# Kernel tuning notes

Measured on AMD Instinct MI355X. Metric: run time of the kernel, lower is better.

The kernel has to match this reference:

```python
import jax, jax.numpy as jnp
import numpy as np

N_NODES, N_EDGES, N_GRAPHS = 8192, 32768, 256
FXD, HEADS = 78, 10
D2 = FXD * HEADS  # 780
FF = 2048
L_MUT = 735
NF = 32
OUT_DIM = 128


def _ln(x, g, b, eps=1e-5):
    m = x.mean(-1, keepdims=True)
    v = ((x - m) ** 2).mean(-1, keepdims=True)
    return (x - m) * jax.lax.rsqrt(v + eps) * g + b


def _transformer(x, in_w, in_b, out_w, out_b, ln1_g, ln1_b, l1_w, l1_b, l2_w, l2_b, ln2_g, ln2_b):
    # post-LN TransformerEncoderLayer, nhead=1, seq = all N nodes, batch = 1 (eval: dropout off)
    E = x.shape[-1]
    q, k, v = jnp.split(x @ in_w.T + in_b, 3, axis=-1)
    a = jax.nn.softmax((q @ k.T) * (1.0 / np.sqrt(E)), axis=-1) @ v  # [N,N] scores
    x = _ln(x + a @ out_w.T + out_b, ln1_g, ln1_b)
    h = jax.nn.relu(x @ l1_w.T + l1_b) @ l2_w.T + l2_b
    return _ln(x + h, ln2_g, ln2_b)


def _gat(x, src, dst, w, a_src, a_dst, bias):
    # PyG GATConv, heads=10, concat=True, leaky 0.2, self loops already in src/dst
    N = x.shape[0]
    h = (x @ w.T).reshape(N, HEADS, FXD)
    asrc = (h * a_src).sum(-1)  # [N,H]
    adst = (h * a_dst).sum(-1)
    alpha = jax.nn.leaky_relu(asrc[src] + adst[dst], 0.2)  # [E,H]
    amax = jax.lax.stop_gradient(jax.ops.segment_max(alpha, dst, num_segments=N))
    ex = jnp.exp(alpha - amax[dst])
    coef = ex / (jax.ops.segment_sum(ex, dst, num_segments=N)[dst] + 1e-16)
    out = jax.ops.segment_sum(coef[:, :, None] * h[src], dst, num_segments=N)
    return out.reshape(N, HEADS * FXD) + bias


def _gcn(x, src, dst, w, b):
    # PyG GCNConv with self loops (already in src/dst), symmetric norm
    N = x.shape[0]
    deg = jax.ops.segment_sum(jnp.ones(dst.shape, x.dtype), dst, num_segments=N)
    dis = jnp.where(deg > 0, jax.lax.rsqrt(jnp.maximum(deg, 1.0)), 0.0)
    norm = dis[src] * dis[dst]
    return jax.ops.segment_sum(norm[:, None] * (x @ w.T)[src], dst, num_segments=N) + b


def _conv1d(x, w, b):
    y = jax.lax.conv_general_dilated(x, w, (1,), 'VALID', dimension_numbers=('NCH', 'OIH', 'NCH'))
    return y + b[None, :, None]


def _convT1d(x, w, b):
    # torch ConvTranspose1d weight [in,out,k] -> flipped [out,in,k], full padding
    k = w.shape[-1]
    ker = jnp.flip(w, -1).transpose(1, 0, 2)
    y = jax.lax.conv_general_dilated(x, ker, (1,), [(k - 1, k - 1)], dimension_numbers=('NCH', 'OIH', 'NCH'))
    return y + b[None, :, None]


def _maxpool1d(x, k):
    return jax.lax.reduce_window(x, -jnp.inf, jax.lax.max, (1, 1, k), (1, 1, k), 'VALID')


def _bn_eval(x, g, b, eps=1e-5):
    # eval-mode BatchNorm1d with fresh running stats (mean 0, var 1)
    return x * (g / np.sqrt(1.0 + eps))[None, :, None] + b[None, :, None]


def _forward(edge_index, batch, x, target_mut, t1_in_w, t1_in_b, t1_out_w, t1_out_b, t1_ln1_g, t1_ln1_b, t1_l1_w, t1_l1_b, t1_l2_w, t1_l2_b, t1_ln2_g, t1_ln2_b, gat_w, gat_asrc, gat_adst, gat_b, t2_in_w, t2_in_b, t2_out_w, t2_out_b, t2_ln1_g, t2_ln1_b, t2_l1_w, t2_l1_b, t2_l2_w, t2_l2_b, t2_ln2_g, t2_ln2_b, gcn_w, gcn_b, fcg1_w, fcg1_b, fcg2_w, fcg2_b, e1_w, e1_b, bn1_g, bn1_b, e2_w, e2_b, bn2_g, bn2_b, e3_w, e3_b, enc_lin_w, enc_lin_b, d3_w, d3_b, dbn2_g, dbn2_b, d2_w, d2_b, dbn1_g, dbn1_b, d1_w, d1_b, fc1_w, fc1_b, fc2_w, fc2_b, out_w, out_b):
    N = x.shape[0]
    xg = _transformer(x, t1_in_w, t1_in_b, t1_out_w, t1_out_b, t1_ln1_g, t1_ln1_b, t1_l1_w, t1_l1_b, t1_l2_w, t1_l2_b, t1_ln2_g, t1_ln2_b)
    loops = jnp.arange(N, dtype=edge_index.dtype)
    src = jnp.concatenate([edge_index[0], loops])
    dst = jnp.concatenate([edge_index[1], loops])
    xg = jax.nn.relu(_gat(xg, src, dst, gat_w, gat_asrc, gat_adst, gat_b))
    xg = _transformer(xg, t2_in_w, t2_in_b, t2_out_w, t2_out_b, t2_ln1_g, t2_ln1_b, t2_l1_w, t2_l1_b, t2_l2_w, t2_l2_b, t2_ln2_g, t2_ln2_b)
    xg = jax.nn.relu(_gcn(xg, src, dst, gcn_w, gcn_b))
    gm = jax.ops.segment_max(xg, batch, num_segments=N_GRAPHS)
    gm = jnp.where(jnp.isfinite(gm), gm, 0.0)
    cnt = jax.ops.segment_sum(jnp.ones((N,), xg.dtype), batch, num_segments=N_GRAPHS)
    ga = jax.ops.segment_sum(xg, batch, num_segments=N_GRAPHS) / jnp.maximum(cnt, 1.0)[:, None]
    xd = jnp.concatenate([gm, ga], axis=1)  # [B, 1560]
    xd = jax.nn.relu(xd @ fcg1_w.T + fcg1_b)
    xd = xd @ fcg2_w.T + fcg2_b  # [B, 128]
    # conv1d autoencoder on mutation profile
    t = target_mut[:, None, :]  # [B,1,735]
    e = jax.nn.leaky_relu(_bn_eval(_maxpool1d(_conv1d(t, e1_w, e1_b), 8), bn1_g, bn1_b))
    e = jax.nn.leaky_relu(_bn_eval(_maxpool1d(_conv1d(e, e2_w, e2_b), 7), bn2_g, bn2_b))
    e = _conv1d(e, e3_w, e3_b)  # [B,128,5]
    z = e.reshape(e.shape[0], -1) @ enc_lin_w.T + enc_lin_b  # [B,128]
    d = jnp.repeat(jax.nn.leaky_relu(_bn_eval(_convT1d(e, d3_w, d3_b), dbn2_g, dbn2_b)), 7, axis=-1)
    d = jnp.repeat(jax.nn.leaky_relu(_bn_eval(_convT1d(d, d2_w, d2_b), dbn1_g, dbn1_b)), 8, axis=-1)
    decode = _convT1d(d, d1_w, d1_b)  # [B,1,735]
    xc = jnp.concatenate([xd, z], axis=1)
    xc = jax.nn.relu(xc @ fc1_w.T + fc1_b)
    xc = jax.nn.relu(xc @ fc2_w.T + fc2_b)
    out = jax.nn.sigmoid(xc @ out_w.T + out_b)
    return (out, xd, decode)


def setup_inputs():
    key = jax.random.key(0)
    ks = iter(jax.random.split(key, 64))

    def rn(*shape):
        return jax.random.normal(next(ks), shape, jnp.float32) * 0.05

    inp = {}
    inp['x'] = jax.random.normal(next(ks), (N_NODES, FXD), jnp.float32)
    inp['edge_index'] = jax.random.randint(next(ks), (2, N_EDGES), 0, N_NODES)
    inp['batch'] = jnp.sort(jax.random.randint(next(ks), (N_NODES,), 0, N_GRAPHS))
    inp['target_mut'] = jax.random.normal(next(ks), (N_GRAPHS, L_MUT), jnp.float32)
    for p, E in (('t1', FXD), ('t2', D2)):
        inp[p + '_in_w'] = rn(3 * E, E); inp[p + '_in_b'] = jnp.zeros((3 * E,))
        inp[p + '_out_w'] = rn(E, E); inp[p + '_out_b'] = jnp.zeros((E,))
        inp[p + '_ln1_g'] = jnp.ones((E,)); inp[p + '_ln1_b'] = jnp.zeros((E,))
        inp[p + '_l1_w'] = rn(FF, E); inp[p + '_l1_b'] = jnp.zeros((FF,))
        inp[p + '_l2_w'] = rn(E, FF); inp[p + '_l2_b'] = jnp.zeros((E,))
        inp[p + '_ln2_g'] = jnp.ones((E,)); inp[p + '_ln2_b'] = jnp.zeros((E,))
    inp['gat_w'] = rn(D2, FXD); inp['gat_asrc'] = rn(HEADS, FXD); inp['gat_adst'] = rn(HEADS, FXD); inp['gat_b'] = jnp.zeros((D2,))
    inp['gcn_w'] = rn(D2, D2); inp['gcn_b'] = jnp.zeros((D2,))
    inp['fcg1_w'] = rn(1500, 2 * D2); inp['fcg1_b'] = jnp.zeros((1500,))
    inp['fcg2_w'] = rn(OUT_DIM, 1500); inp['fcg2_b'] = jnp.zeros((OUT_DIM,))
    inp['e1_w'] = rn(NF, 1, 8); inp['e1_b'] = jnp.zeros((NF,))
    inp['bn1_g'] = jnp.ones((NF,)); inp['bn1_b'] = jnp.zeros((NF,))
    inp['e2_w'] = rn(2 * NF, NF, 8); inp['e2_b'] = jnp.zeros((2 * NF,))
    inp['bn2_g'] = jnp.ones((2 * NF,)); inp['bn2_b'] = jnp.zeros((2 * NF,))
    inp['e3_w'] = rn(4 * NF, 2 * NF, 8); inp['e3_b'] = jnp.zeros((4 * NF,))
    inp['enc_lin_w'] = rn(OUT_DIM, 640); inp['enc_lin_b'] = jnp.zeros((OUT_DIM,))
    inp['d3_w'] = rn(4 * NF, 2 * NF, 8); inp['d3_b'] = jnp.zeros((2 * NF,))
    inp['dbn2_g'] = jnp.ones((2 * NF,)); inp['dbn2_b'] = jnp.zeros((2 * NF,))
    inp['d2_w'] = rn(2 * NF, NF, 8); inp['d2_b'] = jnp.zeros((NF,))
    inp['dbn1_g'] = jnp.ones((NF,)); inp['dbn1_b'] = jnp.zeros((NF,))
    inp['d1_w'] = rn(NF, 1, 8); inp['d1_b'] = jnp.zeros((1,))
    inp['fc1_w'] = rn(1024, 2 * OUT_DIM); inp['fc1_b'] = jnp.zeros((1024,))
    inp['fc2_w'] = rn(128, 1024); inp['fc2_b'] = jnp.zeros((128,))
    inp['out_w'] = rn(1, 128); inp['out_b'] = jnp.zeros((1,))
    return inp


def reference(x, edge_index, batch, target_mut, t1_in_w, t1_in_b, t1_out_w, t1_out_b, t1_ln1_g, t1_ln1_b, t1_l1_w, t1_l1_b, t1_l2_w, t1_l2_b, t1_ln2_g, t1_ln2_b, gat_w, gat_asrc, gat_adst, gat_b, t2_in_w, t2_in_b, t2_out_w, t2_out_b, t2_ln1_g, t2_ln1_b, t2_l1_w, t2_l1_b, t2_l2_w, t2_l2_b, t2_ln2_g, t2_ln2_b, gcn_w, gcn_b, fcg1_w, fcg1_b, fcg2_w, fcg2_b, e1_w, e1_b, bn1_g, bn1_b, e2_w, e2_b, bn2_g, bn2_b, e3_w, e3_b, enc_lin_w, enc_lin_b, d3_w, d3_b, dbn2_g, dbn2_b, d2_w, d2_b, dbn1_g, dbn1_b, d1_w, d1_b, fc1_w, fc1_b, fc2_w, fc2_b, out_w, out_b):
    return _forward(edge_index, batch, x, target_mut, t1_in_w, t1_in_b, t1_out_w, t1_out_b, t1_ln1_g, t1_ln1_b, t1_l1_w, t1_l1_b, t1_l2_w, t1_l2_b, t1_ln2_g, t1_ln2_b, gat_w, gat_asrc, gat_adst, gat_b, t2_in_w, t2_in_b, t2_out_w, t2_out_b, t2_ln1_g, t2_ln1_b, t2_l1_w, t2_l1_b, t2_l2_w, t2_l2_b, t2_ln2_g, t2_ln2_b, gcn_w, gcn_b, fcg1_w, fcg1_b, fcg2_w, fcg2_b, e1_w, e1_b, bn1_g, bn1_b, e2_w, e2_b, bn2_g, bn2_b, e3_w, e3_b, enc_lin_w, enc_lin_b, d3_w, d3_b, dbn2_g, dbn2_b, d2_w, d2_b, dbn1_g, dbn1_b, d1_w, d1_b, fc1_w, fc1_b, fc2_w, fc2_b, out_w, out_b)
```

## Files before the change

### kernel.cpp

```cpp
#include <hip/hip_runtime.h>
#include <math.h>

#define NN     8192
#define NEDGE  32768
#define NETOT  40960
#define NG     256
#define FXD_   78
#define NH     10
#define DD2    780
#define FFD    2048
#define LMUT   735

static inline int cdiv_i(long long a, int b){ return (int)((a + (long long)b - 1) / b); }
static inline int pad32(int x){ return (x + 31) & ~31; }

typedef __attribute__((ext_vector_type(8))) short bf16x8;
typedef __attribute__((ext_vector_type(4))) float f32x4;

static __device__ __forceinline__ unsigned short f2bf(float f){
    unsigned u = __float_as_uint(f);
    u += 0x7FFFu + ((u >> 16) & 1u);
    return (unsigned short)(u >> 16);
}

static __device__ __forceinline__ void gload16(const void* g, void* l){
    __builtin_amdgcn_global_load_lds((const __attribute__((address_space(1))) void*)g,
                                     (__attribute__((address_space(3))) void*)l, 16, 0, 0);
}

__global__ void fill_f32_k(float* __restrict__ p, float v, long long n){
    long long i = (long long)blockIdx.x * 256 + threadIdx.x;
    if (i < n) p[i] = v;
}
__global__ void fill_u32_k(unsigned* __restrict__ p, unsigned v, long long n){
    long long i = (long long)blockIdx.x * 256 + threadIdx.x;
    if (i < n) p[i] = v;
}

__global__ void cvt_pad_k(const float* __restrict__ src, unsigned short* __restrict__ dst,
                          long long n , int C, int lds_, int ldd)
{
    long long i = (long long)blockIdx.x * 256 + threadIdx.x;
    if (i >= n) return;
    int r = (int)(i / ldd), c = (int)(i % ldd);
    dst[i] = (c < C) ? f2bf(src[(size_t)r * lds_ + c]) : (unsigned short)0;
}

__global__ void norm_cvt_k(const float* __restrict__ A4, unsigned short* __restrict__ XB,
                           int E, int Ep)
{
    long long i = (long long)blockIdx.x * 256 + threadIdx.x;
    if (i >= (long long)NN * Ep) return;
    int r = (int)(i / Ep), c = (int)(i % Ep);
    XB[i] = (c < E) ? f2bf(A4[(size_t)r * Ep + c] / A4[(size_t)r * Ep + E]) : (unsigned short)0;
}

__global__ void tr_bf16_k(const unsigned short* __restrict__ src, unsigned short* __restrict__ dst,
                          int R, int C, int lds_, int ldd)
{
    __shared__ unsigned short t[32][33];
    int cb = blockIdx.x * 32, rb = blockIdx.y * 32;
    int tx = threadIdx.x & 31, ty = threadIdx.x >> 5;
#pragma unroll
    for (int i = 0; i < 4; ++i){
        int r = rb + ty + i * 8, c = cb + tx;
        t[ty + i * 8][tx] = (r < R && c < C) ? src[(size_t)r * lds_ + c] : (unsigned short)0;
    }
    __syncthreads();
#pragma unroll
    for (int i = 0; i < 4; ++i){
        int dr = cb + ty + i * 8, dc = rb + tx;
        if (dr < C && dc < R) dst[(size_t)dr * ldd + dc] = t[tx][ty + i * 8];
    }
}

__global__ void qkv_bias_k(const float* __restrict__ b3, float* __restrict__ out, int E, int Ep)
{
    int idx = blockIdx.x * 256 + threadIdx.x;
    if (idx >= 3 * Ep) return;
    int s = idx / Ep, c = idx % Ep;
    out[idx] = (c < E) ? b3[s * E + c] : 0.f;
}

__global__ void bias_add_k(float* __restrict__ X, const float* __restrict__ b, long long n, int cols)
{
    long long i = (long long)blockIdx.x * 256 + threadIdx.x;
    if (i < n) X[i] += b[i % cols];
}

template<int OUTC, int ACT, int SPLITK, int BROW, int BN>
__global__ __launch_bounds__(256) void mgemm_k(
    const unsigned short* __restrict__ A, const unsigned short* __restrict__ B,
    const float* __restrict__ bias, void* __restrict__ Cv,
    int M, int N, int Kp, int lda, int ldb, int ldc, int swz, float escale)
{
    constexpr int NFJ   = BN / 32;
    constexpr int TILEA = 128 * 32;
    constexpr int TILEB = BN * 32;
    __shared__ unsigned short As[2 * TILEA];
    __shared__ unsigned short Bs[2 * TILEB];
    const int tid = threadIdx.x;
    const int lane = tid & 63, wid = tid >> 6;
    const int r16 = lane & 15, q = lane >> 4;
    const int wr = (wid >> 1) * 64, wc = (wid & 1) * (BN / 2);

    const int gx = gridDim.x, gy = gridDim.y;
    const int nwg = gx * gy;
    int orig = swz ? ((int)blockIdx.x * gy + (int)blockIdx.y)
                   : ((int)blockIdx.y * gx + (int)blockIdx.x);
    int q8 = nwg >> 3, r8 = nwg & 7;
    int xcd = orig & 7, kk8 = orig >> 3;
    int wgid = (xcd < r8 ? xcd * (q8 + 1) : r8 * (q8 + 1) + (xcd - r8) * q8) + kk8;
    int bx, by;
    if (swz){ by = wgid % gy; bx = wgid / gy; }
    else    { bx = wgid % gx; by = wgid / gx; }
    const int row0 = by * 128, col0 = bx * BN;

    int kbeg = 0, kend = Kp;
    if (SPLITK > 1){
        int nt_ = Kp >> 5, cpt = (nt_ + SPLITK - 1) / SPLITK;
        kbeg = (int)blockIdx.z * cpt * 32;
        kend = min(Kp, kbeg + cpt * 32);
    }

    const int c0 = wid * 128 + lane;
    const int r0a = c0 >> 2, k0a = (c0 & 3) << 3;
    const size_t gA0 = (size_t)min(row0 + r0a, M - 1) * lda + k0a;
    const size_t gA1 = (size_t)min(row0 + r0a + 16, M - 1) * lda + k0a;
    unsigned short* lA = As + wid * 1024;
    size_t gB0 = 0, gB1 = 0;
    unsigned short* lB;
    if (BN == 128){
        gB0 = (size_t)min(col0 + r0a, N - 1) * ldb + k0a;
        gB1 = (size_t)min(col0 + r0a + 16, N - 1) * ldb + k0a;
        lB = Bs + wid * 1024;
    } else {
        const int cb = wid * 64 + lane;
        const int rb_ = cb >> 2, kb_ = (cb & 3) << 3;
        gB0 = (size_t)min(col0 + rb_, N - 1) * ldb + kb_;
        lB = Bs + wid * 512;
    }

    f32x4 acc[4][NFJ];
#pragma unroll
    for (int i = 0; i < 4; ++i)
#pragma unroll
        for (int j = 0; j < NFJ; ++j){ f32x4 z = {0.f, 0.f, 0.f, 0.f}; acc[i][j] = z; }

    const int nt = (kend - kbeg) >> 5;
    if (nt > 0){
        gload16(A + gA0 + kbeg, lA);
        gload16(A + gA1 + kbeg, lA + 512);
        gload16(B + gB0 + kbeg, lB);
        if (BN == 128) gload16(B + gB1 + kbeg, lB + 512);
        __syncthreads();
        int cur = 0;
        for (int t = 0; t < nt; ++t){
            const int k0 = kbeg + (t << 5);
            if (t + 1 < nt){
                const int kn = k0 + 32, nb = cur ^ 1;
                gload16(A + gA0 + kn, lA + nb * TILEA);
                gload16(A + gA1 + kn, lA + nb * TILEA + 512);
                gload16(B + gB0 + kn, lB + nb * TILEB);
                if (BN == 128) gload16(B + gB1 + kn, lB + nb * TILEB + 512);
            }
            const unsigned short* Ab = As + cur * TILEA;
            const unsigned short* Bb = Bs + cur * TILEB;
            bf16x8 af[4], bfv[NFJ];
#pragma unroll
            for (int f = 0; f < 4; ++f)
                af[f] = *(const bf16x8*)(Ab + (size_t)(wr + f * 16 + r16) * 32 + (q << 3));
#pragma unroll
            for (int f = 0; f < NFJ; ++f)
                bfv[f] = *(const bf16x8*)(Bb + (size_t)(wc + f * 16 + r16) * 32 + (q << 3));
#pragma unroll
            for (int fi = 0; fi < 4; ++fi)
#pragma unroll
                for (int fj = 0; fj < NFJ; ++fj)
                    acc[fi][fj] = __builtin_amdgcn_mfma_f32_16x16x32_bf16(af[fi], bfv[fj], acc[fi][fj], 0, 0, 0);
            __syncthreads();
            cur ^= 1;
        }
    }

    if (OUTC == 1 && SPLITK == 1 && row0 + 128 <= M && col0 + BN <= N && (ldc & 7) == 0){
#pragma unroll
        for (int fi = 0; fi < 4; ++fi)
#pragma unroll
            for (int fj = 0; fj < NFJ; ++fj)
#pragma unroll
                for (int j = 0; j < 4; ++j){
                    int r = wr + fi * 16 + q * 4 + j;
                    int c = wc + fj * 16 + r16;
                    float v = acc[fi][fj][j];
                    if (bias) v += BROW ? bias[row0 + r] : bias[col0 + c];
                    if (ACT == 1) v = fmaxf(v, 0.f);
                    if (ACT == 2) v = 1.f / (1.f + __expf(-v));
                    if (ACT == 3) v = __expf(v * escale);
                    unsigned short* buf = (r < 64) ? As : Bs;
                    buf[(r & 63) * BN + (c ^ ((r & 7) << 3))] = f2bf(v);
                }
        __syncthreads();
        const int CPR = BN / 8;
        for (int id = tid; id < 128 * CPR; id += 256){
            int r = id / CPR, cg = (id % CPR) * 8;
            const unsigned short* buf = (r < 64) ? As : Bs;
            uint4 vv = *(const uint4*)(&buf[(r & 63) * BN + (cg ^ ((r & 7) << 3))]);
            *(uint4*)((unsigned short*)Cv + (size_t)(row0 + r) * ldc + col0 + cg) = vv;
        }
        return;
    }

#pragma unroll
    for (int fi = 0; fi < 4; ++fi){
#pragma unroll
        for (int j = 0; j < 4; ++j){
            int r = row0 + wr + fi * 16 + q * 4 + j;
            if (r >= M) continue;
#pragma unroll
            for (int fj = 0; fj < NFJ; ++fj){
                int c = col0 + wc + fj * 16 + r16;
                if (c >= N) continue;
                float v = acc[fi][fj][j];
                if (SPLITK > 1){
                    atomicAdd((float*)Cv + (size_t)r * ldc + c, v);
                } else {
                    if (bias) v += BROW ? bias[r] : bias[c];
                    if (ACT == 1) v = fmaxf(v, 0.f);
                    if (ACT == 2) v = 1.f / (1.f + __expf(-v));
                    if (ACT == 3) v = __expf(v * escale);
                    if (OUTC == 0) ((float*)Cv)[(size_t)r * ldc + c] = v;
                    else ((unsigned short*)Cv)[(size_t)r * ldc + c] = f2bf(v);
                }
            }
        }
    }
}

template<int OUTC, int ACT, int SPLITK, int BROW, int BN>
static void mgemm(hipStream_t s, const unsigned short* A, const unsigned short* B,
                  const float* bias, void* C, int M, int N, int Kp,
                  int lda, int ldb, int ldc, int swz, float escale = 1.f)
{
    dim3 g(cdiv_i(N, BN), cdiv_i(M, 128), SPLITK);
    mgemm_k<OUTC, ACT, SPLITK, BROW, BN><<<g, 256, 0, s>>>(A, B, bias, C, M, N, Kp, lda, ldb, ldc, swz, escale);
}

#define E3P1 288
#define KLD  104
__global__ __launch_bounds__(256) void flash_t1_k(
    const unsigned short* __restrict__ QKV,
    const unsigned short* __restrict__ Vt,
    float* __restrict__ A4, float scale)
{
    __shared__ unsigned short Ps[128 * 128];
    __shared__ unsigned short Vs[80 * 128];
    const int tid = threadIdx.x, lane = tid & 63, wid = tid >> 6;
    const int r16 = lane & 15, q = lane >> 4;
    const int wr = (wid >> 1) * 64;
    const int sc = (wid & 1) * 64;
    const int oc = (wid & 1) * 48;
    const int NJMAX = (wid & 1) ? 2 : 3;
    const int qb = (int)blockIdx.x * 128;
    const int kb = (int)blockIdx.y * 512;

    bf16x8 qa[4][3];
#pragma unroll
    for (int mi = 0; mi < 4; ++mi)
#pragma unroll
        for (int kc = 0; kc < 3; ++kc)
            qa[mi][kc] = *(const bf16x8*)(QKV + (size_t)(qb + wr + mi * 16 + r16) * E3P1 + kc * 32 + (q << 3));

    f32x4 acco[4][3];
#pragma unroll
    for (int i = 0; i < 4; ++i)
#pragma unroll
        for (int j = 0; j < 3; ++j){ f32x4 z = {0.f, 0.f, 0.f, 0.f}; acco[i][j] = z; }

    for (int t = 0; t < 4; ++t){
        const int k0 = kb + t * 128;
#pragma unroll
        for (int i = 0; i < 6; ++i){
            int id = tid + i * 256;
            int row = id / 12, co = (id % 12) << 3;
            *(bf16x8*)(&Ps[row * KLD + co]) =
                *(const bf16x8*)(QKV + (size_t)(k0 + row) * E3P1 + 96 + co);
        }
        __syncthreads();
        f32x4 accs[4][4];
#pragma unroll
        for (int i = 0; i < 4; ++i)
#pragma unroll
            for (int j = 0; j < 4; ++j){ f32x4 z = {0.f, 0.f, 0.f, 0.f}; accs[i][j] = z; }
#pragma unroll
        for (int kc = 0; kc < 3; ++kc){
            bf16x8 bk[4];
#pragma unroll
            for (int nj = 0; nj < 4; ++nj)
                bk[nj] = *(const bf16x8*)(&Ps[(sc + nj * 16 + r16) * KLD + kc * 32 + (q << 3)]);
#pragma unroll
            for (int mi = 0; mi < 4; ++mi)
#pragma unroll
                for (int nj = 0; nj < 4; ++nj)
                    accs[mi][nj] = __builtin_amdgcn_mfma_f32_16x16x32_bf16(qa[mi][kc], bk[nj], accs[mi][nj], 0, 0, 0);
        }
        __syncthreads();
#pragma unroll
        for (int mi = 0; mi < 4; ++mi)
#pragma unroll
            for (int nj = 0; nj < 4; ++nj)
#pragma unroll
                for (int j = 0; j < 4; ++j){
                    int row = wr + mi * 16 + q * 4 + j;
                    int col = sc + nj * 16 + r16;
                    Ps[row * 128 + (col ^ ((row & 7) << 3))] = f2bf(__expf(accs[mi][nj][j] * scale));
                }
#pragma unroll
        for (int i = 0; i < 5; ++i){
            int id = tid + i * 256;
            int row = id / 16, co = (id % 16) << 3;
            *(bf16x8*)(&Vs[row * 128 + (co ^ ((row & 7) << 3))]) =
                *(const bf16x8*)(Vt + (size_t)row * NN + k0 + co);
        }
        __syncthreads();
#pragma unroll
        for (int ko = 0; ko < 4; ++ko){
            bf16x8 pa[4], vb[3];
#pragma unroll
            for (int mi = 0; mi < 4; ++mi){
                int row = wr + mi * 16 + r16;
                pa[mi] = *(const bf16x8*)(&Ps[row * 128 + ((ko * 32 + (q << 3)) ^ ((row & 7) << 3))]);
            }
#pragma unroll
            for (int nj = 0; nj < 3; ++nj){
                if (nj < NJMAX){
                    int row = oc + nj * 16 + r16;
                    vb[nj] = *(const bf16x8*)(&Vs[row * 128 + ((ko * 32 + (q << 3)) ^ ((row & 7) << 3))]);
                }
            }
#pragma unroll
            for (int mi = 0; mi < 4; ++mi)
#pragma unroll
                for (int nj = 0; nj < 3; ++nj)
                    if (nj < NJMAX)
                        acco[mi][nj] = __builtin_amdgcn_mfma_f32_16x16x32_bf16(pa[mi], vb[nj], acco[mi][nj], 0, 0, 0);
        }
        __syncthreads();
    }
#pragma unroll
    for (int mi = 0; mi < 4; ++mi)
#pragma unroll
        for (int j = 0; j < 4; ++j){
            int r = qb + wr + mi * 16 + q * 4 + j;
#pragma unroll
            for (int nj = 0; nj < 3; ++nj){
                if (nj < NJMAX){
                    int c = oc + nj * 16 + r16;
                    if (c <= FXD_)
                        atomicAdd(A4 + (size_t)r * 96 + c, acco[mi][nj][j]);
                }
            }
        }
}

__global__ __launch_bounds__(256) void add_ln_k(
    const float* __restrict__ X, const float* __restrict__ Y, const float* __restrict__ ybias,
    const float* __restrict__ g, const float* __restrict__ b,
    float* __restrict__ out, unsigned short* __restrict__ obf, int E, int Ep)
{
    __shared__ float s1[256], s2[256];
    const int tid = threadIdx.x;
    long long base = (long long)blockIdx.x * E;
    float vals[4];
    float sum = 0.f, sq = 0.f;
    int i = 0;
    for (int c = tid; c < Ep; c += 256, ++i){
        float v = 0.f;
        if (c < E){
            v = X[base + c] + Y[base + c];
            if (ybias) v += ybias[c];
            sum += v; sq += v * v;
        }
        vals[i] = v;
    }
    s1[tid] = sum; s2[tid] = sq; __syncthreads();
    for (int s = 128; s; s >>= 1){
        if (tid < s){ s1[tid] += s1[tid + s]; s2[tid] += s2[tid + s]; }
        __syncthreads();
    }
    float mean = s1[0] / (float)E;
    float var = s2[0] / (float)E - mean * mean;
    if (var < 0.f) var = 0.f;
    float inv = 1.f / sqrtf(var + 1e-5f);
    i = 0;
    for (int c = tid; c < Ep; c += 256, ++i){
        if (c < E){
            float o = (vals[i] - mean) * inv * g[c] + b[c];
            out[base + c] = o;
            if (obf) obf[(size_t)blockIdx.x * Ep + c] = f2bf(o);
        } else if (obf) obf[(size_t)blockIdx.x * Ep + c] = 0;
    }
}

static __device__ __forceinline__ unsigned enc_f(float x){
    unsigned u = __float_as_uint(x);
    return (u & 0x80000000u) ? ~u : (u | 0x80000000u);
}
static __device__ __forceinline__ float dec_f(unsigned u){
    return (u & 0x80000000u) ? __uint_as_float(u & 0x7fffffffu) : __uint_as_float(~u);
}
static __device__ __forceinline__ void edge_sd(const int* __restrict__ ei, int e, int& s, int& d){
    if (e < NEDGE){ s = ei[e]; d = ei[NEDGE + e]; }
    else { s = e - NEDGE; d = e - NEDGE; }
}

__global__ void gat_srcdst_k(const float* __restrict__ h, const float* __restrict__ aw_src,
                             const float* __restrict__ aw_dst, float* __restrict__ asrc,
                             float* __restrict__ adst)
{
    int idx = blockIdx.x * 256 + threadIdx.x;
    if (idx >= NN * NH) return;
    int n = idx / NH, hh = idx % NH;
    const float* hp = h + (long long)n * DD2 + hh * FXD_;
    const float* ws = aw_src + hh * FXD_;
    const float* wd = aw_dst + hh * FXD_;
    float s1 = 0.f, s2 = 0.f;
    for (int f = 0; f < FXD_; ++f){ float v = hp[f]; s1 += v * ws[f]; s2 += v * wd[f]; }
    asrc[idx] = s1; adst[idx] = s2;
}

__global__ void gat_alpha_k(const int* __restrict__ ei, const float* __restrict__ asrc,
                            const float* __restrict__ adst, float* __restrict__ alpha,
                            unsigned* __restrict__ amax)
{
    int idx = blockIdx.x * 256 + threadIdx.x;
    if (idx >= NETOT * NH) return;
    int e = idx / NH, hh = idx % NH;
    int s, d; edge_sd(ei, e, s, d);
    float a = asrc[s * NH + hh] + adst[d * NH + hh];
    a = (a > 0.f) ? a : 0.2f * a;
    alpha[idx] = a;
    atomicMax(&amax[d * NH + hh], enc_f(a));
}

__global__ void gat_expsum_k(const int* __restrict__ ei, float* __restrict__ alpha,
                             const unsigned* __restrict__ amax, float* __restrict__ denom)
{
    int idx = blockIdx.x * 256 + threadIdx.x;
    if (idx >= NETOT * NH) return;
    int e = idx / NH, hh = idx % NH;
    int s, d; edge_sd(ei, e, s, d);
    float m = dec_f(amax[d * NH + hh]);
    float ex = expf(alpha[idx] - m);
    alpha[idx] = ex;
    atomicAdd(&denom[d * NH + hh], ex);
}

__global__ void deg_count_k(const int* __restrict__ ei, int* __restrict__ deg)
{
    int e = blockIdx.x * 256 + threadIdx.x;
    if (e >= NETOT) return;
    int s, d; edge_sd(ei, e, s, d);
    atomicAdd(&deg[d], 1);
}

__global__ __launch_bounds__(256) void csr_off_k(const int* __restrict__ deg,
                                                 int* __restrict__ off, int* __restrict__ cur)
{
    __shared__ int pref[257];
    const int tid = threadIdx.x;
    int loc[32];
    int base = tid * 32, sum = 0;
#pragma unroll
    for (int i = 0; i < 32; ++i){ loc[i] = sum; sum += deg[base + i]; }
    __shared__ int part[256];
    part[tid] = sum; __syncthreads();
    if (tid == 0){
        pref[0] = 0;
        for (int i = 0; i < 256; ++i) pref[i + 1] = pref[i] + part[i];
    }
    __syncthreads();
    int p0 = pref[tid];
#pragma unroll
    for (int i = 0; i < 32; ++i){ off[base + i] = p0 + loc[i]; cur[base + i] = p0 + loc[i]; }
    if (tid == 0) off[NN] = pref[256];
}

__global__ void csr_fill_k(const int* __restrict__ ei, int* __restrict__ cur,
                           int* __restrict__ csr_s, int* __restrict__ csr_e)
{
    int e = blockIdx.x * 256 + threadIdx.x;
    if (e >= NETOT) return;
    int s, d; edge_sd(ei, e, s, d);
    int pos = atomicAdd(&cur[d], 1);
    csr_s[pos] = s; csr_e[pos] = e;
}

__global__ __launch_bounds__(256) void gat_gather_k(
    const int* __restrict__ off, const int* __restrict__ csr_s, const int* __restrict__ csr_e,
    const float* __restrict__ ex, const float* __restrict__ denom,
    const float* __restrict__ hfeat, float* __restrict__ out)
{
    const int d = blockIdx.x, tid = threadIdx.x;
    const int beg = off[d], end = off[d + 1];
    for (int f = tid; f < DD2; f += 256){
        int hh = f / FXD_;
        float acc = 0.f;
        for (int p = beg; p < end; ++p)
            acc += ex[csr_e[p] * NH + hh] * hfeat[(size_t)csr_s[p] * DD2 + f];
        out[(size_t)d * DD2 + f] = acc / (denom[d * NH + hh] + 1e-16f);
    }
}

__global__ __launch_bounds__(256) void gcn_gather_k(
    const int* __restrict__ off, const int* __restrict__ csr_s,
    const float* __restrict__ dis, const float* __restrict__ xw, float* __restrict__ out)
{
    const int d = blockIdx.x, tid = threadIdx.x;
    const int beg = off[d], end = off[d + 1];
    const float dd_ = dis[d];
    for (int f = tid; f < DD2; f += 256){
        float acc = 0.f;
        for (int p = beg; p < end; ++p){
            int s = csr_s[p];
            acc += dis[s] * xw[(size_t)s * DD2 + f];
        }
        out[(size_t)d * DD2 + f] = acc * dd_;
    }
}

__global__ void bias_relu_k(float* __restrict__ X, const float* __restrict__ b,
                            unsigned short* __restrict__ obf, int rows, int cols, int ldp)
{
    long long i = (long long)blockIdx.x * 256 + threadIdx.x;
    if (i >= (long long)rows * ldp) return;
    int r = (int)(i / ldp), c = (int)(i % ldp);
    if (c < cols){
        float v = X[(size_t)r * cols + c] + b[c];
        v = v > 0.f ? v : 0.f;
        X[(size_t)r * cols + c] = v;
        if (obf) obf[i] = f2bf(v);
    } else if (obf) obf[i] = 0;
}

__global__ void dis_k(const int* __restrict__ deg, float* __restrict__ dis)
{
    int n = blockIdx.x * 256 + threadIdx.x;
    if (n >= NN) return;
    float d = (float)deg[n];
    dis[n] = (d > 0.f) ? 1.f / sqrtf(fmaxf(d, 1.f)) : 0.f;
}

__global__ void seg_start_k(const int* __restrict__ batch, int* __restrict__ start)
{
    int n = blockIdx.x * 256 + threadIdx.x;
    if (n >= NN) return;
    int b = batch[n];
    int bp = (n == 0) ? -1 : batch[n - 1];
    for (int g = bp + 1; g <= b; ++g) start[g] = n;
    if (n == NN - 1){
        for (int g = b + 1; g <= NG; ++g) start[g] = NN;
    }
}

__global__ __launch_bounds__(256) void pool_seg_k(const float* __restrict__ xg,
                                                  const int* __restrict__ start,
                                                  unsigned short* __restrict__ xdb)
{
    const int g = blockIdx.x, tid = threadIdx.x;
    const int s0 = start[g], s1 = start[g + 1];
    const float inv = 1.f / fmaxf((float)(s1 - s0), 1.f);
    for (int f = tid; f < DD2; f += 256){
        float mx = 0.f, sm = 0.f;
        for (int n = s0; n < s1; ++n){
            float v = xg[(size_t)n * DD2 + f];
            mx = fmaxf(mx, v); sm += v;
        }
        xdb[(size_t)g * 1568 + f] = f2bf(mx);
        xdb[(size_t)g * 1568 + DD2 + f] = f2bf(sm * inv);
    }
    if (tid < 8) xdb[(size_t)g * 1568 + 1560 + tid] = 0;
}

#define BN_SCALE 0.9999950000374996f

__global__ __launch_bounds__(256) void enc1_b(const float* __restrict__ tm, const float* __restrict__ w,
                                              const float* __restrict__ bias, const float* __restrict__ bng,
                                              const float* __restrict__ bnb, float* __restrict__ out)
{
    __shared__ float xs[736];
    __shared__ float ws[256], bs[32], gs[32], b2[32];
    const int g = blockIdx.x, tid = threadIdx.x;
    for (int i = tid; i < 735; i += 256) xs[i] = tm[(size_t)g * LMUT + i];
    ws[tid] = w[tid];
    if (tid < 32){ bs[tid] = bias[tid]; gs[tid] = bng[tid]; b2[tid] = bnb[tid]; }
    __syncthreads();
    for (int idx = tid; idx < 32 * 91; idx += 256){
        int o = idx / 91, t = idx % 91;
        float mx = -3.4e38f;
        for (int p = 0; p < 8; ++p){
            float s = bs[o];
#pragma unroll
            for (int k = 0; k < 8; ++k) s += xs[t * 8 + p + k] * ws[o * 8 + k];
            mx = fmaxf(mx, s);
        }
        float v = mx * gs[o] * BN_SCALE + b2[o];
        out[(size_t)g * 2912 + idx] = v > 0.f ? v : 0.01f * v;
    }
}

__global__ void i2c_enc2_k(const float* __restrict__ in, unsigned short* __restrict__ A){
    int idx = blockIdx.x * 256 + threadIdx.x;
    if (idx >= NG * 84 * 256) return;
    int col = idx & 255, row = idx >> 8;
    int g = row / 84, u = row % 84;
    int i = col >> 3, k = col & 7;
    A[idx] = f2bf(in[(size_t)g * 2912 + i * 91 + u + k]);
}
__global__ void post_enc2_k(const float* __restrict__ G, const float* __restrict__ b,
                            const float* __restrict__ bng, const float* __restrict__ bnb,
                            float* __restrict__ out){
    int idx = blockIdx.x * 256 + threadIdx.x;
    if (idx >= NG * 768) return;
    int t = idx % 12, o = (idx / 12) & 63, g = idx / 768;
    float mx = -3.4e38f;
#pragma unroll
    for (int p = 0; p < 7; ++p) mx = fmaxf(mx, G[(size_t)(g * 84 + t * 7 + p) * 64 + o]);
    float v = (mx + b[o]) * bng[o] * BN_SCALE + bnb[o];
    out[(size_t)g * 768 + o * 12 + t] = v > 0.f ? v : 0.01f * v;
}
__global__ void i2c_enc3_k(const float* __restrict__ in, unsigned short* __restrict__ A){
    int idx = blockIdx.x * 256 + threadIdx.x;
    if (idx >= NG * 5 * 512) return;
    int col = idx & 511, row = idx >> 9;
    int g = row / 5, t = row % 5;
    int i2 = col >> 3, k = col & 7;
    A[idx] = f2bf(in[(size_t)g * 768 + i2 * 12 + t + k]);
}
__global__ void post_enc3_k(const float* __restrict__ G, const float* __restrict__ b,
                            float* __restrict__ e3o, unsigned short* __restrict__ obf){
    int idx = blockIdx.x * 256 + threadIdx.x;
    if (idx >= NG * 640) return;
    int t = idx % 5, o = (idx / 5) & 127, g = idx / 640;
    float v = G[(size_t)(g * 5 + t) * 128 + o] + b[o];
    e3o[(size_t)g * 640 + o * 5 + t] = v;
    obf[(size_t)g * 640 + o * 5 + t] = f2bf(v);
}
__global__ void wshuf_k(const float* __restrict__ src, unsigned short* __restrict__ dst, int I, int O){
    int idx = blockIdx.x * 256 + threadIdx.x;
    if (idx >= I * O * 8) return;
    int o = idx / (I * 8), rem = idx % (I * 8);
    int i = rem >> 3, j = rem & 7;
    dst[idx] = f2bf(src[(size_t)(i * O + o) * 8 + j]);
}
__global__ void i2c_dec3_k(const float* __restrict__ e3o, unsigned short* __restrict__ A){
    int idx = blockIdx.x * 256 + threadIdx.x;
    if (idx >= NG * 12 * 1024) return;
    int col = idx & 1023, row = idx >> 10;
    int g = row / 12, t = row % 12;
    int i2 = col >> 3, j = col & 7;
    int tt = t - j;
    A[idx] = (tt >= 0 && tt < 5) ? f2bf(e3o[(size_t)g * 640 + i2 * 5 + tt]) : (unsigned short)0;
}
__global__ void post_dec3_k(const float* __restrict__ G, const float* __restrict__ b,
                            const float* __restrict__ bng, const float* __restrict__ bnb,
                            float* __restrict__ dd3){
    int idx = blockIdx.x * 256 + threadIdx.x;
    if (idx >= NG * 768) return;
    int t = idx % 12, o = (idx / 12) & 63, g = idx / 768;
    float v = (G[(size_t)(g * 12 + t) * 64 + o] + b[o]) * bng[o] * BN_SCALE + bnb[o];
    dd3[(size_t)g * 768 + o * 12 + t] = v > 0.f ? v : 0.01f * v;
}
__global__ void i2c_dec2_k(const float* __restrict__ dd3, unsigned short* __restrict__ A){
    int idx = blockIdx.x * 256 + threadIdx.x;
    if (idx >= NG * 91 * 512) return;
    int col = idx & 511, row = idx >> 9;
    int g = row / 91, t = row % 91;
    int i2 = col >> 3, j = col & 7;
    int tt = t - j;
    A[idx] = (tt >= 0 && tt < 84) ? f2bf(dd3[(size_t)g * 768 + i2 * 12 + tt / 7]) : (unsigned short)0;
}
__global__ void post_dec2_k(const float* __restrict__ G, const float* __restrict__ b,
                            const float* __restrict__ bng, const float* __restrict__ bnb,
                            float* __restrict__ dd2){
    int idx = blockIdx.x * 256 + threadIdx.x;
    if (idx >= NG * 2912) return;
    int t = idx % 91, o = (idx / 91) & 31, g = idx / 2912;
    float v = (G[(size_t)(g * 91 + t) * 32 + o] + b[o]) * bng[o] * BN_SCALE + bnb[o];
    dd2[(size_t)g * 2912 + o * 91 + t] = v > 0.f ? v : 0.01f * v;
}

__global__ __launch_bounds__(256) void dec1_b(const float* __restrict__ dd2, const float* __restrict__ w,
                                              const float* __restrict__ bias, float* __restrict__ out)
{
    __shared__ float d2s[32][91];
    __shared__ float ws[256];
    const int g = blockIdx.x, tid = threadIdx.x;
    const int t0 = (int)blockIdx.y * 245;
    for (int i = tid; i < 32 * 91; i += 256) d2s[i / 91][i % 91] = dd2[(size_t)g * 2912 + i];
    ws[tid] = w[tid];
    __syncthreads();
    if (tid < 245){
        int t = t0 + tid;
        int id8[8]; bool ok[8];
#pragma unroll
        for (int j = 0; j < 8; ++j){
            int tt = t - j;
            ok[j] = (tt >= 0 && tt < 728);
            id8[j] = ok[j] ? (tt >> 3) : 0;
        }
        float s = bias[0];
        for (int i2 = 0; i2 < 32; ++i2){
            const float* wp = ws + i2 * 8;
            float a = 0.f;
#pragma unroll
            for (int j = 0; j < 8; ++j) if (ok[j]) a += d2s[i2][id8[j]] * wp[j];
            s += a;
        }
        out[(size_t)g * 735 + t] = s;
    }
}

__global__ void concat_xc_k(const float* __restrict__ xd, const float* __restrict__ z,
                            unsigned short* __restrict__ xcb)
{
    int idx = blockIdx.x * 256 + threadIdx.x;
    if (idx >= NG * 256) return;
    int g = idx >> 8, c = idx & 255;
    xcb[idx] = f2bf((c < 128) ? xd[g * 128 + c] : z[g * 128 + (c - 128)]);
}

extern "C" void kernel_launch(void* const* d_in, const int* in_sizes, int n_in,
                              void* d_out, int out_size, void* d_ws, size_t ws_size,
                              hipStream_t stream)
{
    (void)in_sizes; (void)n_in; (void)out_size;

    const float* x      = (const float*)d_in[0];
    const int*   ei     = (const int*)  d_in[1];
    const int*   batch  = (const int*)  d_in[2];
    const float* tmut   = (const float*)d_in[3];
    const float* t1w[12]; for (int i = 0; i < 12; ++i) t1w[i] = (const float*)d_in[4 + i];
    const float* t2w[12]; for (int i = 0; i < 12; ++i) t2w[i] = (const float*)d_in[16 + i];
    const float* gat_w    = (const float*)d_in[28];
    const float* gat_asrc = (const float*)d_in[29];
    const float* gat_adst = (const float*)d_in[30];
    const float* gat_b    = (const float*)d_in[31];
    const float* gcn_w  = (const float*)d_in[32];
    const float* gcn_b  = (const float*)d_in[33];
    const float* fcg1_w = (const float*)d_in[34];
    const float* fcg1_b = (const float*)d_in[35];
    const float* fcg2_w = (const float*)d_in[36];
    const float* fcg2_b = (const float*)d_in[37];
    const float* e1_w = (const float*)d_in[38]; const float* e1_b = (const float*)d_in[39];
    const float* bn1_g = (const float*)d_in[40]; const float* bn1_b = (const float*)d_in[41];
    const float* e2_w = (const float*)d_in[42]; const float* e2_b = (const float*)d_in[43];
    const float* bn2_g = (const float*)d_in[44]; const float* bn2_b = (const float*)d_in[45];
    const float* e3_w = (const float*)d_in[46]; const float* e3_b = (const float*)d_in[47];
    const float* enc_w = (const float*)d_in[48]; const float* enc_b = (const float*)d_in[49];
    const float* d3_w = (const float*)d_in[50]; const float* d3_b = (const float*)d_in[51];
    const float* dbn2_g = (const float*)d_in[52]; const float* dbn2_b = (const float*)d_in[53];
    const float* d2_w = (const float*)d_in[54]; const float* d2_b = (const float*)d_in[55];
    const float* dbn1_g = (const float*)d_in[56]; const float* dbn1_b = (const float*)d_in[57];
    const float* d1_w = (const float*)d_in[58]; const float* d1_b = (const float*)d_in[59];
    const float* fc1_w = (const float*)d_in[60]; const float* fc1_b = (const float*)d_in[61];
    const float* fc2_w = (const float*)d_in[62]; const float* fc2_b = (const float*)d_in[63];
    const float* outw = (const float*)d_in[64]; const float* outb = (const float*)d_in[65];

    float *A1, *A2, *A3, *A4, *X1f, *QBIASf;
    unsigned short *XB, *QKVb, *Vt, *HbPb;
    unsigned short *WQKVb, *WOUTb, *WL1b, *WL2b, *WGb, *WGCNb, *WFCG1b, *WFCG2b,
                   *WENCb, *WFC1b, *WFC2b, *WOUTWb, *XD16, *FG1b, *E3b, *XCb, *FH1b, *FH2b, *Wcvb;
    float *asrc, *adst, *alpha, *denom, *dis, *c1p, *c2p, *e3o, *zz, *dd3, *dd2b;
    unsigned *amax; int *deg, *seg, *csr_off, *csr_cur, *csr_s, *csr_e;

    auto carve = [&](long long RB) -> size_t {
        char* wp_ = (char*)d_ws;
        auto alc = [&](size_t bytes) -> char* {
            char* p = wp_;
            wp_ += (bytes + 255) & ~(size_t)255;
            return p;
        };
        A1 = (float*)alc((size_t)NN * DD2 * 4);
        A2 = (float*)alc((size_t)NN * DD2 * 4);
        A3 = (float*)alc((size_t)NN * DD2 * 4);
        A4 = (float*)alc((size_t)NN * 800 * 4);
        X1f = (float*)alc((size_t)NN * FXD_ * 4);
        XB   = (unsigned short*)alc((size_t)NN * 800 * 2);
        QKVb = (unsigned short*)alc((size_t)NN * 2400 * 2);
        Vt   = (unsigned short*)alc((size_t)801 * NN * 2);
        size_t hb = (size_t)NN * FFD * 2, pb = (size_t)RB * NN * 2;
        HbPb = (unsigned short*)alc(hb > pb ? hb : pb);
        WQKVb = (unsigned short*)alc((size_t)2400 * 800 * 2);
        QBIASf= (float*)alc((size_t)2400 * 4);
        WOUTb = (unsigned short*)alc((size_t)780 * 800 * 2);
        WL1b  = (unsigned short*)alc((size_t)2048 * 800 * 2);
        WL2b  = (unsigned short*)alc((size_t)780 * 2048 * 2);
        WGb   = (unsigned short*)alc((size_t)780 * 96 * 2);
        WGCNb = (unsigned short*)alc((size_t)780 * 800 * 2);
        WFCG1b= (unsigned short*)alc((size_t)1500 * 1568 * 2);
        WFCG2b= (unsigned short*)alc((size_t)128 * 1504 * 2);
        WENCb = (unsigned short*)alc((size_t)128 * 640 * 2);
        WFC1b = (unsigned short*)alc((size_t)1024 * 256 * 2);
        WFC2b = (unsigned short*)alc((size_t)128 * 1024 * 2);
        WOUTWb= (unsigned short*)alc((size_t)128 * 2);
        Wcvb  = (unsigned short*)alc((size_t)128 * 1024 * 2);
        XD16  = (unsigned short*)alc((size_t)NG * 1568 * 2);
        FG1b  = (unsigned short*)alc((size_t)NG * 1504 * 2);
        E3b   = (unsigned short*)alc((size_t)NG * 640 * 2);
        XCb   = (unsigned short*)alc((size_t)NG * 256 * 2);
        FH1b  = (unsigned short*)alc((size_t)NG * 1024 * 2);
        FH2b  = (unsigned short*)alc((size_t)NG * 128 * 2);
        asrc = (float*)alc((size_t)NN * NH * 4);
        adst = (float*)alc((size_t)NN * NH * 4);
        alpha= (float*)alc((size_t)NETOT * NH * 4);
        amax = (unsigned*)alc((size_t)NN * NH * 4);
        denom= (float*)alc((size_t)NN * NH * 4);
        deg  = (int*)alc((size_t)NN * 4);
        dis  = (float*)alc((size_t)NN * 4);
        seg  = (int*)alc((size_t)(NG + 1) * 4);
        csr_off = (int*)alc((size_t)(NN + 1) * 4);
        csr_cur = (int*)alc((size_t)NN * 4);
        csr_s   = (int*)alc((size_t)NETOT * 4);
        csr_e   = (int*)alc((size_t)NETOT * 4);
        c1p  = (float*)alc((size_t)NG * 32 * 91 * 4);
        c2p  = (float*)alc((size_t)NG * 64 * 12 * 4);
        e3o  = (float*)alc((size_t)NG * 128 * 5 * 4);
        zz   = (float*)alc((size_t)NG * 128 * 4);
        dd3  = (float*)alc((size_t)NG * 64 * 12 * 4);
        dd2b = (float*)alc((size_t)NG * 32 * 91 * 4);
        return (size_t)(wp_ - (char*)d_ws);
    };

    long long RB = 512;
    const long long cands[3] = {2048, 1024, 512};
    for (int i = 0; i < 3; ++i){ if (carve(cands[i]) <= ws_size){ RB = cands[i]; break; } }
    carve(RB);
    unsigned short* Pb = HbPb;
    unsigned short* AIM = HbPb;

    float* out0   = (float*)d_out;
    float* xd_out = (float*)d_out + NG;
    float* decode = (float*)d_out + NG + NG * 128;

    auto cvt = [&](const float* src, unsigned short* dst, int R, int C, int lds_, int ldd){
        long long n = (long long)R * ldd;
        cvt_pad_k<<<cdiv_i(n, 256), 256, 0, stream>>>(src, dst, n, C, lds_, ldd);
    };
    auto zero16 = [&](unsigned short* p, long long nshorts){
        fill_u32_k<<<cdiv_i(nshorts / 2, 256), 256, 0, stream>>>((unsigned*)p, 0u, nshorts / 2);
    };
    auto zerof = [&](float* p, long long n){
        fill_f32_k<<<cdiv_i(n, 256), 256, 0, stream>>>(p, 0.f, n);
    };

    auto run_tf = [&](const float* xin, const float* const* W, float* outp, int E){
        const int Ep = pad32(E), E3p = 3 * Ep;
        float scale = (float)(1.0 / sqrt((double)E));
        zero16(WQKVb, (long long)E3p * Ep);
        for (int s = 0; s < 3; ++s)
            cvt(W[0] + (size_t)s * E * E, WQKVb + (size_t)s * Ep * Ep, E, E, E, Ep);
        qkv_bias_k<<<cdiv_i(E3p, 256), 256, 0, stream>>>(W[1], QBIASf, E, Ep);
        mgemm<1,0,1,0,128>(stream, XB, WQKVb, QBIASf, QKVb, NN, E3p, Ep, Ep, Ep, E3p, 0);
        {
            dim3 g(cdiv_i(E, 32), cdiv_i(NN, 32));
            tr_bf16_k<<<g, 256, 0, stream>>>(QKVb + 2 * Ep, Vt, NN, E, E3p, NN);
            fill_u32_k<<<cdiv_i(NN / 2, 256), 256, 0, stream>>>((unsigned*)(Vt + (size_t)E * NN),
                                                                0x3F803F80u, NN / 2);
        }
        zerof(A4, (long long)NN * Ep);
        if (E == FXD_){
            dim3 g(NN / 128, 16);
            flash_t1_k<<<g, 256, 0, stream>>>(QKVb, Vt, A4, scale);
        } else {
            for (long long r0 = 0; r0 < NN; r0 += RB){
                mgemm<1,3,1,0,128>(stream, QKVb + (size_t)r0 * E3p, QKVb + Ep, nullptr, Pb,
                                   (int)RB, NN, Ep, E3p, E3p, NN, 1, scale);
                mgemm<0,0,4,0,64>(stream, Pb, Vt, nullptr, A4 + (size_t)r0 * Ep,
                                  (int)RB, E + 1, NN, NN, NN, Ep, 0);
            }
        }
        norm_cvt_k<<<cdiv_i((long long)NN * Ep, 256), 256, 0, stream>>>(A4, XB, E, Ep);
        cvt(W[2], WOUTb, E, E, E, Ep);
        mgemm<0,0,1,0,64>(stream, XB, WOUTb, W[3], A2, NN, E, Ep, Ep, Ep, E, 0);
        add_ln_k<<<NN, 256, 0, stream>>>(xin, A2, nullptr, W[4], W[5], A3, XB, E, Ep);
        cvt(W[6], WL1b, FFD, E, E, Ep);
        mgemm<1,1,1,0,128>(stream, XB, WL1b, W[7], HbPb, NN, FFD, Ep, Ep, Ep, FFD, 0);
        cvt(W[8], WL2b, E, FFD, FFD, FFD);
        mgemm<0,0,1,0,64>(stream, HbPb, WL2b, W[9], A2, NN, E, FFD, FFD, FFD, E, 0);
        add_ln_k<<<NN, 256, 0, stream>>>(A3, A2, nullptr, W[10], W[11], outp, XB, E, Ep);
    };

    cvt(x, XB, NN, FXD_, FXD_, 96);
    run_tf(x, t1w, X1f, FXD_);

    fill_u32_k<<<cdiv_i(NN, 256), 256, 0, stream>>>((unsigned*)deg, 0u, NN);
    deg_count_k<<<cdiv_i(NETOT, 256), 256, 0, stream>>>(ei, deg);
    csr_off_k<<<1, 256, 0, stream>>>(deg, csr_off, csr_cur);
    csr_fill_k<<<cdiv_i(NETOT, 256), 256, 0, stream>>>(ei, csr_cur, csr_s, csr_e);
    seg_start_k<<<cdiv_i(NN, 256), 256, 0, stream>>>(batch, seg);

    cvt(gat_w, WGb, DD2, FXD_, FXD_, 96);
    mgemm<0,0,1,0,64>(stream, XB, WGb, nullptr, A2, NN, DD2, 96, 96, 96, DD2, 0);
    gat_srcdst_k<<<cdiv_i((long long)NN * NH, 256), 256, 0, stream>>>(A2, gat_asrc, gat_adst, asrc, adst);
    fill_u32_k<<<cdiv_i((long long)NN * NH, 256), 256, 0, stream>>>(amax, 0x007FFFFFu, (long long)NN * NH);
    zerof(denom, (long long)NN * NH);
    gat_alpha_k<<<cdiv_i((long long)NETOT * NH, 256), 256, 0, stream>>>(ei, asrc, adst, alpha, amax);
    gat_expsum_k<<<cdiv_i((long long)NETOT * NH, 256), 256, 0, stream>>>(ei, alpha, amax, denom);
    gat_gather_k<<<NN, 256, 0, stream>>>(csr_off, csr_s, csr_e, alpha, denom, A2, A1);
    bias_relu_k<<<cdiv_i((long long)NN * 800, 256), 256, 0, stream>>>(A1, gat_b, XB, NN, DD2, 800);

    run_tf(A1, t2w, A1, DD2);

    dis_k<<<cdiv_i(NN, 256), 256, 0, stream>>>(deg, dis);
    cvt(gcn_w, WGCNb, DD2, DD2, DD2, 800);
    mgemm<0,0,1,0,64>(stream, XB, WGCNb, nullptr, A2, NN, DD2, 800, 800, 800, DD2, 0);
    gcn_gather_k<<<NN, 256, 0, stream>>>(csr_off, csr_s, dis, A2, A3);
    bias_relu_k<<<cdiv_i((long long)NN * DD2, 256), 256, 0, stream>>>(A3, gcn_b, nullptr, NN, DD2, DD2);

    pool_seg_k<<<NG, 256, 0, stream>>>(A3, seg, XD16);
    cvt(fcg1_w, WFCG1b, 1500, 1560, 1560, 1568);
    zerof(A2, (long long)NG * 1500);
    mgemm<0,0,8,0,64>(stream, XD16, WFCG1b, nullptr, A2, NG, 1500, 1568, 1568, 1568, 1500, 0);
    bias_relu_k<<<cdiv_i((long long)NG * 1504, 256), 256, 0, stream>>>(A2, fcg1_b, FG1b, NG, 1500, 1504);
    cvt(fcg2_w, WFCG2b, 128, 1500, 1500, 1504);
    zerof(xd_out, (long long)NG * 128);
    mgemm<0,0,16,0,128>(stream, FG1b, WFCG2b, nullptr, xd_out, NG, 128, 1504, 1504, 1504, 128, 0);
    bias_add_k<<<cdiv_i((long long)NG * 128, 256), 256, 0, stream>>>(xd_out, fcg2_b, (long long)NG * 128, 128);

    enc1_b<<<NG, 256, 0, stream>>>(tmut, e1_w, e1_b, bn1_g, bn1_b, c1p);
    i2c_enc2_k<<<cdiv_i((long long)NG * 84 * 256, 256), 256, 0, stream>>>(c1p, AIM);
    cvt(e2_w, Wcvb, 64, 256, 256, 256);
    mgemm<0,0,1,0,64>(stream, AIM, Wcvb, nullptr, A2, NG * 84, 64, 256, 256, 256, 64, 0);
    post_enc2_k<<<cdiv_i((long long)NG * 768, 256), 256, 0, stream>>>(A2, e2_b, bn2_g, bn2_b, c2p);
    i2c_enc3_k<<<cdiv_i((long long)NG * 5 * 512, 256), 256, 0, stream>>>(c2p, AIM);
    cvt(e3_w, Wcvb, 128, 512, 512, 512);
    zerof(A2, (long long)NG * 5 * 128);
    mgemm<0,0,4,0,128>(stream, AIM, Wcvb, nullptr, A2, NG * 5, 128, 512, 512, 512, 128, 0);
    post_enc3_k<<<cdiv_i((long long)NG * 640, 256), 256, 0, stream>>>(A2, e3_b, e3o, E3b);
    cvt(enc_w, WENCb, 128, 640, 640, 640);
    mgemm<0,0,1,0,128>(stream, E3b, WENCb, enc_b, zz, NG, 128, 640, 640, 640, 128, 0);

    wshuf_k<<<cdiv_i(128 * 64 * 8, 256), 256, 0, stream>>>(d3_w, Wcvb, 128, 64);
    i2c_dec3_k<<<cdiv_i((long long)NG * 12 * 1024, 256), 256, 0, stream>>>(e3o, AIM);
    zerof(A2, (long long)NG * 12 * 64);
    mgemm<0,0,4,0,64>(stream, AIM, Wcvb, nullptr, A2, NG * 12, 64, 1024, 1024, 1024, 64, 0);
    post_dec3_k<<<cdiv_i((long long)NG * 768, 256), 256, 0, stream>>>(A2, d3_b, dbn2_g, dbn2_b, dd3);
    wshuf_k<<<cdiv_i(64 * 32 * 8, 256), 256, 0, stream>>>(d2_w, Wcvb, 64, 32);
    i2c_dec2_k<<<cdiv_i((long long)NG * 91 * 512, 256), 256, 0, stream>>>(dd3, AIM);
    mgemm<0,0,1,0,64>(stream, AIM, Wcvb, nullptr, A2, NG * 91, 32, 512, 512, 512, 32, 0);
    post_dec2_k<<<cdiv_i((long long)NG * 2912, 256), 256, 0, stream>>>(A2, d2_b, dbn1_g, dbn1_b, dd2b);
    { dim3 g(NG, 3); dec1_b<<<g, 256, 0, stream>>>(dd2b, d1_w, d1_b, decode); }

    concat_xc_k<<<cdiv_i((long long)NG * 256, 256), 256, 0, stream>>>(xd_out, zz, XCb);
    cvt(fc1_w, WFC1b, 1024, 256, 256, 256);
    mgemm<1,1,1,0,128>(stream, XCb, WFC1b, fc1_b, FH1b, NG, 1024, 256, 256, 256, 1024, 0);
    cvt(fc2_w, WFC2b, 128, 1024, 1024, 1024);
    zerof(A3, (long long)NG * 128);
    mgemm<0,0,8,0,128>(stream, FH1b, WFC2b, nullptr, A3, NG, 128, 1024, 1024, 1024, 128, 0);
    bias_relu_k<<<cdiv_i((long long)NG * 128, 256), 256, 0, stream>>>(A3, fc2_b, FH2b, NG, 128, 128);
    cvt(outw, WOUTWb, 1, 128, 128, 128);
    mgemm<0,2,1,0,64>(stream, FH2b, WOUTWb, outb, out0, NG, 1, 128, 128, 128, 1, 0);
}
```

Measured before the change: 1.470 ms.

## Triple-buffer GEMM shared-memory tiles with explicit vmcnt waits

```diff
diff --git a/kernel.cpp b/kernel.cpp
--- a/kernel.cpp
+++ b/kernel.cpp
@@ -97,8 +97,8 @@
     constexpr int NFJ   = BN / 32;
     constexpr int TILEA = 128 * 32;
     constexpr int TILEB = BN * 32;
-    __shared__ unsigned short As[2 * TILEA];
-    __shared__ unsigned short Bs[2 * TILEB];
+    __shared__ unsigned short As[3 * TILEA];
+    __shared__ unsigned short Bs[3 * TILEB];
     const int tid = threadIdx.x;
     const int lane = tid & 63, wid = tid >> 6;
     const int r16 = lane & 15, q = lane >> 4;
@@ -149,23 +149,33 @@
 
     const int nt = (kend - kbeg) >> 5;
     if (nt > 0){
-        gload16(A + gA0 + kbeg, lA);
-        gload16(A + gA1 + kbeg, lA + 512);
-        gload16(B + gB0 + kbeg, lB);
-        if (BN == 128) gload16(B + gB1 + kbeg, lB + 512);
-        __syncthreads();
-        int cur = 0;
+        auto STAGE = [&](int t, int b){
+            const int ko = kbeg + (t << 5);
+            gload16(A + gA0 + ko, lA + b * TILEA);
+            gload16(A + gA1 + ko, lA + b * TILEA + 512);
+            gload16(B + gB0 + ko, lB + b * TILEB);
+            if (BN == 128) gload16(B + gB1 + ko, lB + b * TILEB + 512);
+        };
+        STAGE(0, 0);
+        if (nt > 1){
+            STAGE(1, 1);
+            if constexpr (BN == 128) asm volatile("s_waitcnt vmcnt(4)" ::: "memory");
+            else                     asm volatile("s_waitcnt vmcnt(3)" ::: "memory");
+        } else {
+            asm volatile("s_waitcnt vmcnt(0)" ::: "memory");
+        }
+        __builtin_amdgcn_s_barrier();
+        __builtin_amdgcn_sched_barrier(0);
+
+        int bcur = 0;
         for (int t = 0; t < nt; ++t){
-            const int k0 = kbeg + (t << 5);
-            if (t + 1 < nt){
-                const int kn = k0 + 32, nb = cur ^ 1;
-                gload16(A + gA0 + kn, lA + nb * TILEA);
-                gload16(A + gA1 + kn, lA + nb * TILEA + 512);
-                gload16(B + gB0 + kn, lB + nb * TILEB);
-                if (BN == 128) gload16(B + gB1 + kn, lB + nb * TILEB + 512);
+            const bool more = (t + 2 < nt);
+            if (more){
+                int b2 = bcur + 2; if (b2 >= 3) b2 -= 3;
+                STAGE(t + 2, b2);
             }
-            const unsigned short* Ab = As + cur * TILEA;
-            const unsigned short* Bb = Bs + cur * TILEB;
+            const unsigned short* Ab = As + bcur * TILEA;
+            const unsigned short* Bb = Bs + bcur * TILEB;
             bf16x8 af[4], bfv[NFJ];
 #pragma unroll
             for (int f = 0; f < 4; ++f)
@@ -178,8 +188,15 @@
 #pragma unroll
                 for (int fj = 0; fj < NFJ; ++fj)
                     acc[fi][fj] = __builtin_amdgcn_mfma_f32_16x16x32_bf16(af[fi], bfv[fj], acc[fi][fj], 0, 0, 0);
-            __syncthreads();
-            cur ^= 1;
+            if (more){
+                if constexpr (BN == 128) asm volatile("s_waitcnt vmcnt(4)" ::: "memory");
+                else                     asm volatile("s_waitcnt vmcnt(3)" ::: "memory");
+            } else {
+                asm volatile("s_waitcnt vmcnt(0)" ::: "memory");
+            }
+            __builtin_amdgcn_s_barrier();
+            __builtin_amdgcn_sched_barrier(0);
+            bcur = (bcur + 1 == 3) ? 0 : bcur + 1;
         }
     }
 
```

New measurement: 1.475 ms. No clear change (+0.3%).
